# Kernel tuning notes

Hardware: AMD Instinct MI355X
Metric: run time of the kernel (lower is better)

Reference implementation:

```python
import jax, jax.numpy as jnp
import numpy as np

N_NODES = 100000
N_EDGES = 1600000
D = 128
N_LAYERS = 3  # GIN num_layers = n_layers + 1 with n_layers = 2
BN_EPS = 1e-5


def _batchnorm(x, gamma, beta):
    # Training-mode BatchNorm1d over the node axis (biased variance, as torch uses
    # for normalization).
    mean = jnp.mean(x, axis=0)
    var = jnp.mean((x - mean) ** 2, axis=0)
    return (x - mean) * jax.lax.rsqrt(var + BN_EPS) * gamma + beta


def setup_inputs() -> dict:
    key = jax.random.key(0)
    ks = jax.random.split(key, 5)
    features = jax.random.normal(ks[0], (N_NODES, D), dtype=jnp.float32)
    W = jax.random.normal(ks[1], (N_LAYERS, D, D), dtype=jnp.float32) * 0.05
    b = jnp.zeros((N_LAYERS, D), dtype=jnp.float32)
    eps = jnp.zeros((N_LAYERS,), dtype=jnp.float32)  # learn_eps init 0
    bn1_gamma = jnp.ones((N_LAYERS, D), dtype=jnp.float32)
    bn1_beta = jnp.zeros((N_LAYERS, D), dtype=jnp.float32)
    bn2_gamma = jnp.ones((N_LAYERS, D), dtype=jnp.float32)
    bn2_beta = jnp.zeros((N_LAYERS, D), dtype=jnp.float32)
    src = jax.random.randint(ks[2], (N_EDGES,), 0, N_NODES, dtype=jnp.int64 if jax.config.jax_enable_x64 else jnp.int32)
    dst = jax.random.randint(ks[3], (N_EDGES,), 0, N_NODES, dtype=jnp.int64 if jax.config.jax_enable_x64 else jnp.int32)
    return {
        'features': features, 'W': W, 'b': b, 'eps': eps,
        'bn1_gamma': bn1_gamma, 'bn1_beta': bn1_beta,
        'bn2_gamma': bn2_gamma, 'bn2_beta': bn2_beta,
        'src': src, 'dst': dst,
    }


def reference(features, W, b, eps, bn1_gamma, bn1_beta, bn2_gamma, bn2_beta, src, dst):
    n = features.shape[0]
    h = features
    hidden_rep = [h]
    for i in range(N_LAYERS):
        # GINConv, 'sum' aggregation: (1+eps)*h_v + sum_{u->v} h_u
        agg = jax.ops.segment_sum(h[src], dst, num_segments=n)
        z = (1.0 + eps[i]) * h + agg
        # ApplyNodeFunc: Linear (num_mlp_layers=1) -> BN -> ReLU
        z = z @ W[i] + b[i]
        z = jax.nn.relu(_batchnorm(z, bn1_gamma[i], bn1_beta[i]))
        # GIN.forward: outer BN -> ReLU
        z = jax.nn.relu(_batchnorm(z, bn2_gamma[i], bn2_beta[i]))
        h = z
        hidden_rep.append(h)
    # torch.stack(hidden_rep) -> [n_layers+2, N, D]
    return jnp.stack(hidden_rep, axis=0)
```

## Files before the change

kernel.cpp:

```cpp
#include <hip/hip_runtime.h>
#include <hip/hip_bf16.h>

#define DD 128

typedef __attribute__((ext_vector_type(8))) short bfrag8;
typedef __attribute__((ext_vector_type(4))) float f32x4;

__device__ __forceinline__ float bf16lo(unsigned int u) {
    union { unsigned int i; float f; } c; c.i = u << 16; return c.f;
}
__device__ __forceinline__ float bf16hi(unsigned int u) {
    union { unsigned int i; float f; } c; c.i = u & 0xffff0000u; return c.f;
}
__device__ __forceinline__ unsigned short f2bf(float f) {
    union { float f; unsigned int i; } c; c.f = f;
    unsigned int x = c.i;
    unsigned int r = (x + 0x7fffu + ((x >> 16) & 1u)) >> 16;
    return (unsigned short)r;
}

__global__ void k_hist(const int* __restrict__ dst, int* __restrict__ deg, int E) {
    int i = blockIdx.x * blockDim.x + threadIdx.x;
    if (i < E) atomicAdd(&deg[dst[i]], 1);
}

__global__ void k_scan1(const int* __restrict__ deg, int* __restrict__ partials, int Nn) {
    __shared__ int s[1024];
    int i = blockIdx.x * 1024 + threadIdx.x;
    s[threadIdx.x] = (i < Nn) ? deg[i] : 0;
    __syncthreads();
    for (int off = 512; off > 0; off >>= 1) {
        if (threadIdx.x < off) s[threadIdx.x] += s[threadIdx.x + off];
        __syncthreads();
    }
    if (threadIdx.x == 0) partials[blockIdx.x] = s[0];
}

__global__ void k_scan2(const int* __restrict__ partials, int* __restrict__ pscan, int nb) {
    if (threadIdx.x == 0) {
        int acc = 0;
        for (int i = 0; i < nb; i++) { pscan[i] = acc; acc += partials[i]; }
    }
}

__global__ void k_scan3(const int* __restrict__ deg, const int* __restrict__ pscan,
                        int* __restrict__ row_start, int Nn, int E) {
    __shared__ int s[1024];
    int i = blockIdx.x * 1024 + threadIdx.x;
    int v = (i < Nn) ? deg[i] : 0;
    s[threadIdx.x] = v;
    __syncthreads();
    for (int off = 1; off < 1024; off <<= 1) {
        int t = (threadIdx.x >= off) ? s[threadIdx.x - off] : 0;
        __syncthreads();
        s[threadIdx.x] += t;
        __syncthreads();
    }
    if (i < Nn) row_start[i] = pscan[blockIdx.x] + s[threadIdx.x] - v;
    if (blockIdx.x == 0 && threadIdx.x == 0) row_start[Nn] = E;
}

__global__ void k_scatter(const int* __restrict__ src, const int* __restrict__ dst,
                          const int* __restrict__ row_start, int* __restrict__ cursor,
                          int* __restrict__ csr, int E) {
    int i = blockIdx.x * blockDim.x + threadIdx.x;
    if (i < E) {
        int d = dst[i];
        int pos = row_start[d] + atomicAdd(&cursor[d], 1);
        csr[pos] = src[i];
    }
}

__global__ void k_cvt_feat(const float* __restrict__ f, float* __restrict__ out0,
                           unsigned int* __restrict__ hb, int total4) {
    int i = blockIdx.x * blockDim.x + threadIdx.x;
    if (i >= total4) return;
    float4 v = ((const float4*)f)[i];
    ((float4*)out0)[i] = v;
    unsigned int lo = (unsigned int)f2bf(v.x) | ((unsigned int)f2bf(v.y) << 16);
    unsigned int hi = (unsigned int)f2bf(v.z) | ((unsigned int)f2bf(v.w) << 16);
    ((uint2*)hb)[i] = make_uint2(lo, hi);
}

__global__ void k_cvtW(const float* __restrict__ W, unsigned short* __restrict__ Wt, int total) {
    int i = blockIdx.x * blockDim.x + threadIdx.x;
    if (i >= total) return;
    int l = i >> 14;
    int r = i & 16383;
    int k = r >> 7, n = r & 127;
    Wt[(l << 14) + n * 128 + k] = f2bf(W[i]);
}

__global__ void k_gather(const unsigned int* __restrict__ hb, const int* __restrict__ row_start,
                         const int* __restrict__ csr, const float* __restrict__ eps, int layer,
                         unsigned int* __restrict__ zb, int Nn) {
    int wv = threadIdx.x >> 6, lane = threadIdx.x & 63;
    int v = blockIdx.x * 4 + wv;
    if (v >= Nn) return;
    float e1 = 1.0f + eps[layer];
    unsigned int hs = hb[v * 64 + lane];
    float ax = e1 * bf16lo(hs);
    float ay = e1 * bf16hi(hs);
    int beg = row_start[v], end = row_start[v + 1];
    int e = beg;
    for (; e + 3 < end; e += 4) {
        int u0 = csr[e], u1 = csr[e + 1], u2 = csr[e + 2], u3 = csr[e + 3];
        unsigned int h0 = hb[u0 * 64 + lane];
        unsigned int h1 = hb[u1 * 64 + lane];
        unsigned int h2 = hb[u2 * 64 + lane];
        unsigned int h3 = hb[u3 * 64 + lane];
        ax += bf16lo(h0) + bf16lo(h1) + bf16lo(h2) + bf16lo(h3);
        ay += bf16hi(h0) + bf16hi(h1) + bf16hi(h2) + bf16hi(h3);
    }
    for (; e < end; e++) {
        unsigned int hu = hb[csr[e] * 64 + lane];
        ax += bf16lo(hu); ay += bf16hi(hu);
    }
    zb[v * 64 + lane] = (unsigned int)f2bf(ax) | ((unsigned int)f2bf(ay) << 16);
}

__launch_bounds__(256)
__global__ void k_gemm(const unsigned short* __restrict__ zb, const unsigned short* __restrict__ Wt,
                       const float* __restrict__ bias, int layer, float* __restrict__ y,
                       float* __restrict__ s1sum, float* __restrict__ s1sq, int Nn) {
    __shared__ unsigned short Al[64 * 136];
    __shared__ unsigned short Bl[128 * 136];
    int tid = threadIdx.x;
    int m0 = blockIdx.x * 64;
    const unsigned short* Wl = Wt + (layer << 14);
    #pragma unroll
    for (int p = 0; p < 8; p++) {
        int slot = p * 256 + tid;
        int n = slot >> 4, c = slot & 15;
        *(uint4*)&Bl[n * 136 + c * 8] = *(const uint4*)&Wl[n * 128 + c * 8];
    }
    #pragma unroll
    for (int p = 0; p < 4; p++) {
        int slot = p * 256 + tid;
        int r = slot >> 4, c = slot & 15;
        int grow = m0 + r;
        uint4 val = make_uint4(0, 0, 0, 0);
        if (grow < Nn) val = *(const uint4*)&zb[(size_t)grow * 128 + c * 8];
        *(uint4*)&Al[r * 136 + c * 8] = val;
    }
    __syncthreads();

    int lane = tid & 63, wv = tid >> 6;
    int tcol = lane & 15, quad = lane >> 4;
    f32x4 acc[4][2];
    #pragma unroll
    for (int a = 0; a < 4; a++)
        #pragma unroll
        for (int b2 = 0; b2 < 2; b2++) acc[a][b2] = (f32x4){0.f, 0.f, 0.f, 0.f};

    #pragma unroll
    for (int kk = 0; kk < 128; kk += 32) {
        int kb = kk + quad * 8;
        bfrag8 af[4], bf[2];
        #pragma unroll
        for (int mt = 0; mt < 4; mt++)
            af[mt] = *(const bfrag8*)&Al[(16 * mt + tcol) * 136 + kb];
        #pragma unroll
        for (int nt = 0; nt < 2; nt++)
            bf[nt] = *(const bfrag8*)&Bl[(32 * wv + 16 * nt + tcol) * 136 + kb];
        #pragma unroll
        for (int mt = 0; mt < 4; mt++)
            #pragma unroll
            for (int nt = 0; nt < 2; nt++)
                acc[mt][nt] = __builtin_amdgcn_mfma_f32_16x16x32_bf16(af[mt], bf[nt], acc[mt][nt], 0, 0, 0);
    }

    #pragma unroll
    for (int nt = 0; nt < 2; nt++) {
        int col = 32 * wv + 16 * nt + tcol;
        float bcol = bias[layer * 128 + col];
        float psum = 0.f, psq = 0.f;
        #pragma unroll
        for (int mt = 0; mt < 4; mt++) {
            #pragma unroll
            for (int r = 0; r < 4; r++) {
                int row = m0 + 16 * mt + quad * 4 + r;
                float val = acc[mt][nt][r] + bcol;
                if (row < Nn) {
                    y[(size_t)row * 128 + col] = val;
                    psum += val;
                    psq += val * val;
                }
            }
        }
        psum += __shfl_xor(psum, 16); psq += __shfl_xor(psq, 16);
        psum += __shfl_xor(psum, 32); psq += __shfl_xor(psq, 32);
        if (lane < 16) {
            atomicAdd(&s1sum[col], psum);
            atomicAdd(&s1sq[col], psq);
        }
    }
}

__global__ void k_fin(float* __restrict__ sum, float* __restrict__ sq,
                      const float* __restrict__ gamma, const float* __restrict__ beta, int layer,
                      float* __restrict__ sc, float* __restrict__ sh, float invN) {
    int c = threadIdx.x;
    float m = sum[c] * invN;
    float var = sq[c] * invN - m * m;
    float rstd = rsqrtf(var + 1e-5f);
    float s = gamma[layer * 128 + c] * rstd;
    sc[c] = s;
    sh[c] = beta[layer * 128 + c] - m * s;
    sum[c] = 0.f;
    sq[c] = 0.f;
}

__global__ void k_stats2(const float* __restrict__ y, const float* __restrict__ s1,
                         const float* __restrict__ sh1, float* __restrict__ s2sum,
                         float* __restrict__ s2sq, int Nn) {
    int c = threadIdx.x & 127;
    int r0 = blockIdx.x * 2 + (threadIdx.x >> 7);
    float sc = s1[c], sh = sh1[c];
    float sum = 0.f, sq = 0.f;
    int stride = gridDim.x * 2;
    for (int r = r0; r < Nn; r += stride) {
        float t = fmaxf(y[(size_t)r * 128 + c] * sc + sh, 0.f);
        sum += t;
        sq += t * t;
    }
    atomicAdd(&s2sum[c], sum);
    atomicAdd(&s2sq[c], sq);
}

__global__ void k_apply(float* __restrict__ y, const float* __restrict__ s1,
                        const float* __restrict__ sh1, const float* __restrict__ s2,
                        const float* __restrict__ sh2, unsigned int* __restrict__ hb, int total4) {
    int i = blockIdx.x * blockDim.x + threadIdx.x;
    if (i >= total4) return;
    int c = (i * 4) & 127;
    float4 v = ((float4*)y)[i];
    float t0 = fmaxf(v.x * s1[c] + sh1[c], 0.f);
    float t1 = fmaxf(v.y * s1[c + 1] + sh1[c + 1], 0.f);
    float t2 = fmaxf(v.z * s1[c + 2] + sh1[c + 2], 0.f);
    float t3 = fmaxf(v.w * s1[c + 3] + sh1[c + 3], 0.f);
    float o0 = fmaxf(t0 * s2[c] + sh2[c], 0.f);
    float o1 = fmaxf(t1 * s2[c + 1] + sh2[c + 1], 0.f);
    float o2 = fmaxf(t2 * s2[c + 2] + sh2[c + 2], 0.f);
    float o3 = fmaxf(t3 * s2[c + 3] + sh2[c + 3], 0.f);
    ((float4*)y)[i] = make_float4(o0, o1, o2, o3);
    unsigned int lo = (unsigned int)f2bf(o0) | ((unsigned int)f2bf(o1) << 16);
    unsigned int hi = (unsigned int)f2bf(o2) | ((unsigned int)f2bf(o3) << 16);
    ((uint2*)hb)[i] = make_uint2(lo, hi);
}

extern "C" void kernel_launch(void* const* d_in, const int* in_sizes, int n_in,
                              void* d_out, int out_size, void* d_ws, size_t ws_size,
                              hipStream_t stream) {
    const float* features = (const float*)d_in[0];
    const float* W        = (const float*)d_in[1];
    const float* bias     = (const float*)d_in[2];
    const float* eps      = (const float*)d_in[3];
    const float* g1       = (const float*)d_in[4];
    const float* b1       = (const float*)d_in[5];
    const float* g2       = (const float*)d_in[6];
    const float* b2       = (const float*)d_in[7];
    const int*   src      = (const int*)d_in[8];
    const int*   dst      = (const int*)d_in[9];

    const int Nn = in_sizes[0] / DD;
    const int E  = in_sizes[8];
    const int L  = 3;
    float* out = (float*)d_out;

    char* w = (char*)d_ws;
    auto alloc = [&](size_t bytes) -> char* {
        char* p = w;
        w += (bytes + 255) & ~(size_t)255;
        return p;
    };
    int* deg       = (int*)alloc((size_t)Nn * 4);
    int* cursor    = (int*)alloc((size_t)Nn * 4);
    int* row_start = (int*)alloc((size_t)(Nn + 1) * 4);
    int* partials  = (int*)alloc(1024);
    int* pscan     = (int*)alloc(1024);
    int* csr       = (int*)alloc((size_t)E * 4);
    unsigned int* hb = (unsigned int*)alloc((size_t)Nn * 64 * 4);
    unsigned int* zb = (unsigned int*)alloc((size_t)Nn * 64 * 4);
    unsigned short* Wt = (unsigned short*)alloc((size_t)3 * 128 * 128 * 2);
    float* s1sum = (float*)alloc(512);
    float* s1sq  = (float*)alloc(512);
    float* s2sum = (float*)alloc(512);
    float* s2sq  = (float*)alloc(512);
    float* s1    = (float*)alloc(512);
    float* sh1   = (float*)alloc(512);
    float* s2    = (float*)alloc(512);
    float* sh2   = (float*)alloc(512);

    hipMemsetAsync(deg, 0, (size_t)Nn * 4, stream);
    hipMemsetAsync(cursor, 0, (size_t)Nn * 4, stream);
    hipMemsetAsync(s1sum, 0, 4 * 512, stream);

    const int nb = (Nn + 1023) / 1024;
    k_hist<<<(E + 255) / 256, 256, 0, stream>>>(dst, deg, E);
    k_scan1<<<nb, 1024, 0, stream>>>(deg, partials, Nn);
    k_scan2<<<1, 64, 0, stream>>>(partials, pscan, nb);
    k_scan3<<<nb, 1024, 0, stream>>>(deg, pscan, row_start, Nn, E);
    k_scatter<<<(E + 255) / 256, 256, 0, stream>>>(src, dst, row_start, cursor, csr, E);

    const int total4 = Nn * DD / 4;
    k_cvt_feat<<<(total4 + 255) / 256, 256, 0, stream>>>(features, out, hb, total4);
    k_cvtW<<<(3 * 128 * 128 + 255) / 256, 256, 0, stream>>>(W, Wt, 3 * 128 * 128);

    const float invN = 1.0f / (float)Nn;
    for (int l = 0; l < L; l++) {
        float* y = out + (size_t)(l + 1) * Nn * DD;
        k_gather<<<(Nn + 3) / 4, 256, 0, stream>>>(hb, row_start, csr, eps, l, zb, Nn);
        k_gemm<<<(Nn + 63) / 64, 256, 0, stream>>>((const unsigned short*)zb, Wt, bias, l, y,
                                                   s1sum, s1sq, Nn);
        k_fin<<<1, 128, 0, stream>>>(s1sum, s1sq, g1, b1, l, s1, sh1, invN);
        k_stats2<<<512, 256, 0, stream>>>(y, s1, sh1, s2sum, s2sq, Nn);
        k_fin<<<1, 128, 0, stream>>>(s2sum, s2sq, g2, b2, l, s2, sh2, invN);
        k_apply<<<(total4 + 255) / 256, 256, 0, stream>>>(y, s1, sh1, s2, sh2, hb, total4);
    }
}
```

Baseline: 991.3 us.

## Fuse whole GIN pipeline into one cooperative persistent kernel with grid syncs

Replaces the sequence of about two dozen kernel launches (CSR build, conversions, per-layer gather, GEMM, BN stats, apply) with a single cooperative kernel that uses grid.sync between phases. The gather now writes its aggregated rows straight into shared memory and feeds the MFMA GEMM in the same tile loop, which removes the zb round trip through global memory. The scan is restructured to use per-512-node chunks plus chunk offsets. This trades launch overhead and intermediate traffic for grid-wide barriers, a persistent grid capped at 3 blocks per CU, and a separate fp32 y buffer. The old multi-kernel path is kept as a fallback if the cooperative launch fails.

Measured after the change: 2.030 ms. +104.7%, slower.

```diff
diff --git a/kernel.cpp b/kernel.cpp
--- a/kernel.cpp
+++ b/kernel.cpp
@@ -1,5 +1,8 @@
 #include <hip/hip_runtime.h>
 #include <hip/hip_bf16.h>
+#include <hip/hip_cooperative_groups.h>
+
+namespace cg = cooperative_groups;
 
 #define DD 128
 
@@ -17,6 +20,277 @@
     unsigned int x = c.i;
     unsigned int r = (x + 0x7fffu + ((x >> 16) & 1u)) >> 16;
     return (unsigned short)r;
+}
+
+struct MegaArgs {
+    const float *features, *W, *bias, *eps, *g1, *b1, *g2, *b2;
+    const int *src, *dst;
+    float* out;
+    int Nn, E, ntiles, nchunk, total4;
+    float invN;
+    int *deg, *cursor, *row_local, *partials, *pscan, *csr;
+    unsigned int* hb;
+    unsigned short* Wt;
+    float* y;
+    float* stats;
+};
+
+__launch_bounds__(256, 3)
+__global__ void k_mega(MegaArgs a) {
+    cg::grid_group grid = cg::this_grid();
+    __shared__ __align__(16) char smem[52224];
+    unsigned short* wl = (unsigned short*)smem;
+    unsigned short* zl = (unsigned short*)(smem + 34816);
+    int*   scani = (int*)(smem + 34816);
+    float* red   = (float*)(smem + 34816);
+
+    const int tid  = threadIdx.x;
+    const int bid  = blockIdx.x;
+    const int nb   = gridDim.x;
+    const int gsz  = nb * 256;
+    const int gtid = bid * 256 + tid;
+    const int lane = tid & 63, wv = tid >> 6;
+
+    for (int i = gtid; i < a.Nn; i += gsz) { a.deg[i] = 0; a.cursor[i] = 0; }
+    for (int i = gtid; i < 3 * 512; i += gsz) a.stats[i] = 0.f;
+    grid.sync();
+
+    for (int i = gtid; i < a.E; i += gsz) atomicAdd(&a.deg[a.dst[i]], 1);
+    for (int i = gtid; i < a.total4; i += gsz) {
+        float4 v = ((const float4*)a.features)[i];
+        ((float4*)a.out)[i] = v;
+        unsigned int lo = (unsigned int)f2bf(v.x) | ((unsigned int)f2bf(v.y) << 16);
+        unsigned int hi = (unsigned int)f2bf(v.z) | ((unsigned int)f2bf(v.w) << 16);
+        ((uint2*)a.hb)[i] = make_uint2(lo, hi);
+    }
+    for (int i = gtid; i < 3 * 128 * 128; i += gsz) {
+        int l = i >> 14, r = i & 16383, k = r >> 7, n = r & 127;
+        a.Wt[(l << 14) + n * 128 + k] = f2bf(a.W[i]);
+    }
+    grid.sync();
+
+    for (int c = bid; c < a.nchunk; c += nb) {
+        int base = c << 9;
+        int i0 = base + 2 * tid, i1 = i0 + 1;
+        int d0 = (i0 < a.Nn) ? a.deg[i0] : 0;
+        int d1 = (i1 < a.Nn) ? a.deg[i1] : 0;
+        scani[tid] = d0 + d1;
+        __syncthreads();
+        for (int off = 1; off < 256; off <<= 1) {
+            int t = (tid >= off) ? scani[tid - off] : 0;
+            __syncthreads();
+            scani[tid] += t;
+            __syncthreads();
+        }
+        int incl = scani[tid];
+        int excl = incl - d0 - d1;
+        if (i0 < a.Nn) a.row_local[i0] = excl;
+        if (i1 < a.Nn) a.row_local[i1] = excl + d0;
+        if (tid == 255) a.partials[c] = incl;
+        __syncthreads();
+    }
+    grid.sync();
+
+    if (bid == 0) {
+        int p = (tid < a.nchunk) ? a.partials[tid] : 0;
+        scani[tid] = p;
+        __syncthreads();
+        for (int off = 1; off < 256; off <<= 1) {
+            int t = (tid >= off) ? scani[tid - off] : 0;
+            __syncthreads();
+            scani[tid] += t;
+            __syncthreads();
+        }
+        if (tid < a.nchunk) a.pscan[tid] = scani[tid] - p;
+    }
+    grid.sync();
+
+    for (int i = gtid; i < a.E; i += gsz) {
+        int d = a.dst[i];
+        int pos = a.row_local[d] + a.pscan[d >> 9] + atomicAdd(&a.cursor[d], 1);
+        a.csr[pos] = a.src[i];
+    }
+    grid.sync();
+
+    for (int l = 0; l < 3; ++l) {
+        float* stl = a.stats + l * 512;
+
+        const unsigned short* Wl = a.Wt + (l << 14);
+        for (int i = tid; i < 2048; i += 256) {
+            int n = i >> 4, c = i & 15;
+            *(uint4*)&wl[n * 136 + c * 8] = *(const uint4*)&Wl[n * 128 + c * 8];
+        }
+        float e1v = 1.0f + a.eps[l];
+        __syncthreads();
+
+        for (int t = bid; t < a.ntiles; t += nb) {
+            int m0 = t << 6;
+            for (int rr = wv; rr < 64; rr += 4) {
+                int v = m0 + rr;
+                unsigned int packed = 0;
+                if (v < a.Nn) {
+                    unsigned int hs = a.hb[(size_t)v * 64 + lane];
+                    float ax = e1v * bf16lo(hs), ay = e1v * bf16hi(hs);
+                    int beg = a.row_local[v] + a.pscan[v >> 9];
+                    int vn = v + 1;
+                    int end = (vn < a.Nn) ? (a.row_local[vn] + a.pscan[vn >> 9]) : a.E;
+                    int e = beg;
+                    for (; e + 3 < end; e += 4) {
+                        int u0 = a.csr[e], u1 = a.csr[e + 1], u2 = a.csr[e + 2], u3 = a.csr[e + 3];
+                        unsigned int h0 = a.hb[(size_t)u0 * 64 + lane];
+                        unsigned int h1 = a.hb[(size_t)u1 * 64 + lane];
+                        unsigned int h2 = a.hb[(size_t)u2 * 64 + lane];
+                        unsigned int h3 = a.hb[(size_t)u3 * 64 + lane];
+                        ax += bf16lo(h0) + bf16lo(h1) + bf16lo(h2) + bf16lo(h3);
+                        ay += bf16hi(h0) + bf16hi(h1) + bf16hi(h2) + bf16hi(h3);
+                    }
+                    for (; e < end; ++e) {
+                        unsigned int hu = a.hb[(size_t)a.csr[e] * 64 + lane];
+                        ax += bf16lo(hu); ay += bf16hi(hu);
+                    }
+                    packed = (unsigned int)f2bf(ax) | ((unsigned int)f2bf(ay) << 16);
+                }
+                ((unsigned int*)&zl[rr * 136])[lane] = packed;
+            }
+            __syncthreads();
+
+            int tcol = lane & 15, quad = lane >> 4;
+            f32x4 acc[4][2];
+            #pragma unroll
+            for (int m = 0; m < 4; m++)
+                #pragma unroll
+                for (int n = 0; n < 2; n++) acc[m][n] = (f32x4){0.f, 0.f, 0.f, 0.f};
+            #pragma unroll
+            for (int kk = 0; kk < 128; kk += 32) {
+                int kb = kk + quad * 8;
+                bfrag8 af[4], bf[2];
+                #pragma unroll
+                for (int mt = 0; mt < 4; mt++)
+                    af[mt] = *(const bfrag8*)&zl[(16 * mt + tcol) * 136 + kb];
+                #pragma unroll
+                for (int nt = 0; nt < 2; nt++)
+                    bf[nt] = *(const bfrag8*)&wl[(32 * wv + 16 * nt + tcol) * 136 + kb];
+                #pragma unroll
+                for (int mt = 0; mt < 4; mt++)
+                    #pragma unroll
+                    for (int nt = 0; nt < 2; nt++)
+                        acc[mt][nt] = __builtin_amdgcn_mfma_f32_16x16x32_bf16(af[mt], bf[nt], acc[mt][nt], 0, 0, 0);
+            }
+
+            #pragma unroll
+            for (int nt = 0; nt < 2; nt++) {
+                int col = 32 * wv + 16 * nt + tcol;
+                float bcol = a.bias[l * 128 + col];
+                float psum = 0.f, psq = 0.f;
+                #pragma unroll
+                for (int mt = 0; mt < 4; mt++) {
+                    #pragma unroll
+                    for (int r = 0; r < 4; r++) {
+                        int row = m0 + 16 * mt + quad * 4 + r;
+                        float val = acc[mt][nt][r] + bcol;
+                        if (row < a.Nn) {
+                            a.y[(size_t)row * 128 + col] = val;
+                            psum += val;
+                            psq += val * val;
+                        }
+                    }
+                }
+                psum += __shfl_xor(psum, 16); psq += __shfl_xor(psq, 16);
+                psum += __shfl_xor(psum, 32); psq += __shfl_xor(psq, 32);
+                if (lane < 16) {
+                    atomicAdd(&stl[col], psum);
+                    atomicAdd(&stl[128 + col], psq);
+                }
+            }
+            __syncthreads();
+        }
+        grid.sync();
+
+        if (tid < 128) {
+            float m = stl[tid] * a.invN;
+            float var = stl[128 + tid] * a.invN - m * m;
+            float rstd = rsqrtf(var + 1e-5f);
+            float s = a.g1[l * 128 + tid] * rstd;
+            red[tid] = s;
+            red[128 + tid] = a.b1[l * 128 + tid] - m * s;
+            red[256 + tid] = 0.f;
+            red[384 + tid] = 0.f;
+        }
+        __syncthreads();
+        int cbase = (4 * lane) & 127;
+        float s1r[4], sh1r[4];
+        #pragma unroll
+        for (int j = 0; j < 4; j++) { s1r[j] = red[cbase + j]; sh1r[j] = red[128 + cbase + j]; }
+        float ps[4] = {0.f, 0.f, 0.f, 0.f}, pq[4] = {0.f, 0.f, 0.f, 0.f};
+        for (int i = gtid; i < a.total4; i += gsz) {
+            float4 v = ((const float4*)a.y)[i];
+            float t0 = fmaxf(v.x * s1r[0] + sh1r[0], 0.f);
+            float t1 = fmaxf(v.y * s1r[1] + sh1r[1], 0.f);
+            float t2 = fmaxf(v.z * s1r[2] + sh1r[2], 0.f);
+            float t3 = fmaxf(v.w * s1r[3] + sh1r[3], 0.f);
+            ps[0] += t0; pq[0] += t0 * t0;
+            ps[1] += t1; pq[1] += t1 * t1;
+            ps[2] += t2; pq[2] += t2 * t2;
+            ps[3] += t3; pq[3] += t3 * t3;
+        }
+        #pragma unroll
+        for (int j = 0; j < 4; j++) {
+            ps[j] += __shfl_xor(ps[j], 32);
+            pq[j] += __shfl_xor(pq[j], 32);
+        }
+        if (lane < 32) {
+            #pragma unroll
+            for (int j = 0; j < 4; j++) {
+                atomicAdd(&red[256 + cbase + j], ps[j]);
+                atomicAdd(&red[384 + cbase + j], pq[j]);
+            }
+        }
+        __syncthreads();
+        if (tid < 128) {
+            atomicAdd(&stl[256 + tid], red[256 + tid]);
+            atomicAdd(&stl[384 + tid], red[384 + tid]);
+        }
+        grid.sync();
+
+        if (tid < 128) {
+            float m1 = stl[tid] * a.invN;
+            float v1 = stl[128 + tid] * a.invN - m1 * m1;
+            float r1 = rsqrtf(v1 + 1e-5f);
+            float s1 = a.g1[l * 128 + tid] * r1;
+            red[tid] = s1;
+            red[128 + tid] = a.b1[l * 128 + tid] - m1 * s1;
+            float m2 = stl[256 + tid] * a.invN;
+            float v2 = stl[384 + tid] * a.invN - m2 * m2;
+            float r2 = rsqrtf(v2 + 1e-5f);
+            float s2 = a.g2[l * 128 + tid] * r2;
+            red[256 + tid] = s2;
+            red[384 + tid] = a.b2[l * 128 + tid] - m2 * s2;
+        }
+        __syncthreads();
+        float s1a[4], sh1a[4], s2a[4], sh2a[4];
+        #pragma unroll
+        for (int j = 0; j < 4; j++) {
+            s1a[j]  = red[cbase + j];       sh1a[j] = red[128 + cbase + j];
+            s2a[j]  = red[256 + cbase + j]; sh2a[j] = red[384 + cbase + j];
+        }
+        float* outl = a.out + (size_t)(l + 1) * a.Nn * DD;
+        for (int i = gtid; i < a.total4; i += gsz) {
+            float4 v = ((const float4*)a.y)[i];
+            float t0 = fmaxf(v.x * s1a[0] + sh1a[0], 0.f);
+            float t1 = fmaxf(v.y * s1a[1] + sh1a[1], 0.f);
+            float t2 = fmaxf(v.z * s1a[2] + sh1a[2], 0.f);
+            float t3 = fmaxf(v.w * s1a[3] + sh1a[3], 0.f);
+            float o0 = fmaxf(t0 * s2a[0] + sh2a[0], 0.f);
+            float o1 = fmaxf(t1 * s2a[1] + sh2a[1], 0.f);
+            float o2 = fmaxf(t2 * s2a[2] + sh2a[2], 0.f);
+            float o3 = fmaxf(t3 * s2a[3] + sh2a[3], 0.f);
+            ((float4*)outl)[i] = make_float4(o0, o1, o2, o3);
+            unsigned int lo = (unsigned int)f2bf(o0) | ((unsigned int)f2bf(o1) << 16);
+            unsigned int hi = (unsigned int)f2bf(o2) | ((unsigned int)f2bf(o3) << 16);
+            ((uint2*)a.hb)[i] = make_uint2(lo, hi);
+        }
+        grid.sync();
+    }
 }
 
 __global__ void k_hist(const int* __restrict__ dst, int* __restrict__ deg, int E) {
@@ -265,7 +539,6 @@
 
     const int Nn = in_sizes[0] / DD;
     const int E  = in_sizes[8];
-    const int L  = 3;
     float* out = (float*)d_out;
 
     char* w = (char*)d_ws;
@@ -283,32 +556,59 @@
     unsigned int* hb = (unsigned int*)alloc((size_t)Nn * 64 * 4);
     unsigned int* zb = (unsigned int*)alloc((size_t)Nn * 64 * 4);
     unsigned short* Wt = (unsigned short*)alloc((size_t)3 * 128 * 128 * 2);
-    float* s1sum = (float*)alloc(512);
-    float* s1sq  = (float*)alloc(512);
-    float* s2sum = (float*)alloc(512);
-    float* s2sq  = (float*)alloc(512);
+    float* yb   = (float*)alloc((size_t)Nn * 128 * 4);
+    float* stats = (float*)alloc(3 * 512 * 4);
     float* s1    = (float*)alloc(512);
     float* sh1   = (float*)alloc(512);
     float* s2    = (float*)alloc(512);
     float* sh2   = (float*)alloc(512);
 
+    const int total4 = Nn * DD / 4;
+    const float invN = 1.0f / (float)Nn;
+
+    MegaArgs ma;
+    ma.features = features; ma.W = W; ma.bias = bias; ma.eps = eps;
+    ma.g1 = g1; ma.b1 = b1; ma.g2 = g2; ma.b2 = b2;
+    ma.src = src; ma.dst = dst; ma.out = out;
+    ma.Nn = Nn; ma.E = E;
+    ma.ntiles = (Nn + 63) / 64;
+    ma.nchunk = (Nn + 511) / 512;
+    ma.total4 = total4;
+    ma.invN = invN;
+    ma.deg = deg; ma.cursor = cursor; ma.row_local = row_start;
+    ma.partials = partials; ma.pscan = pscan; ma.csr = csr;
+    ma.hb = hb; ma.Wt = Wt; ma.y = yb; ma.stats = stats;
+
+    int occ = 0;
+    hipError_t oe = hipOccupancyMaxActiveBlocksPerMultiprocessor(&occ, (const void*)k_mega, 256, 0);
+    int bpc = (oe == hipSuccess && occ > 0) ? occ : 2;
+    if (bpc > 3) bpc = 3;
+    int grid = 256 * bpc;
+
+    void* kargs[] = { &ma };
+    hipError_t err = hipLaunchCooperativeKernel((void*)k_mega, dim3(grid), dim3(256),
+                                                kargs, 0, stream);
+    if (err == hipSuccess) return;
+
     hipMemsetAsync(deg, 0, (size_t)Nn * 4, stream);
     hipMemsetAsync(cursor, 0, (size_t)Nn * 4, stream);
-    hipMemsetAsync(s1sum, 0, 4 * 512, stream);
+    hipMemsetAsync(stats, 0, 3 * 512 * 4, stream);
 
     const int nb = (Nn + 1023) / 1024;
+    float* s1sum = stats;
+    float* s1sq  = stats + 128;
+    float* s2sum = stats + 256;
+    float* s2sq  = stats + 384;
+
     k_hist<<<(E + 255) / 256, 256, 0, stream>>>(dst, deg, E);
     k_scan1<<<nb, 1024, 0, stream>>>(deg, partials, Nn);
     k_scan2<<<1, 64, 0, stream>>>(partials, pscan, nb);
     k_scan3<<<nb, 1024, 0, stream>>>(deg, pscan, row_start, Nn, E);
     k_scatter<<<(E + 255) / 256, 256, 0, stream>>>(src, dst, row_start, cursor, csr, E);
-
-    const int total4 = Nn * DD / 4;
     k_cvt_feat<<<(total4 + 255) / 256, 256, 0, stream>>>(features, out, hb, total4);
     k_cvtW<<<(3 * 128 * 128 + 255) / 256, 256, 0, stream>>>(W, Wt, 3 * 128 * 128);
 
-    const float invN = 1.0f / (float)Nn;
-    for (int l = 0; l < L; l++) {
+    for (int l = 0; l < 3; l++) {
         float* y = out + (size_t)(l + 1) * Nn * DD;
         k_gather<<<(Nn + 3) / 4, 256, 0, stream>>>(hb, row_start, csr, eps, l, zb, Nn);
         k_gemm<<<(Nn + 63) / 64, 256, 0, stream>>>((const unsigned short*)zb, Wt, bias, l, y,
```
